# Performance work log

Hardware: AMD Instinct MI355X
Metric: run time of the kernel (lower is better)

The kernel has to match this reference:

```python
import jax, jax.numpy as jnp
import numpy as np

NU, NI, DIN, DH, L, NNZ = 100000, 50000, 64, 128, 2, 5000000
SLOPE = 0.2  # LeakyReLU negative slope (args['p'])
EPS = 1e-5


def setup_inputs() -> dict:
    key = jax.random.key(0)
    ks = jax.random.split(key, 10)
    return {
        'emb_table': jax.random.normal(ks[0], (NU + NI, DIN), jnp.float32) * 0.1,
        'fc_u_w': jax.random.normal(ks[1], (DH, DIN), jnp.float32) * 0.01,
        'fc_u_b': jnp.zeros((DH,), jnp.float32),
        'fc_i_w': jax.random.normal(ks[2], (DH, DIN), jnp.float32) * 0.01,
        'fc_i_b': jnp.zeros((DH,), jnp.float32),
        'vals': jax.random.uniform(ks[3], (NNZ,), jnp.float32),
        'Wu': jax.random.normal(ks[4], (L, DH, DH), jnp.float32) * 0.01,
        'ln1g_u': jnp.ones((L, DH), jnp.float32),
        'ln1b_u': jnp.zeros((L, DH), jnp.float32),
        'ln2g_u': jnp.ones((L, DH), jnp.float32),
        'ln2b_u': jnp.zeros((L, DH), jnp.float32),
        'Wi': jax.random.normal(ks[5], (L, DH, DH), jnp.float32) * 0.01,
        'ln1g_i': jnp.ones((L, DH), jnp.float32),
        'ln1b_i': jnp.zeros((L, DH), jnp.float32),
        'ln2g_i': jnp.ones((L, DH), jnp.float32),
        'ln2b_i': jnp.zeros((L, DH), jnp.float32),
        'rows': jax.random.randint(ks[6], (NNZ,), 0, NU, jnp.int32),
        'cols': jax.random.randint(ks[7], (NNZ,), 0, NI, jnp.int32),
    }


def layer_norm(x, g, b):
    mu = jnp.mean(x, axis=-1, keepdims=True)
    xc = x - mu
    var = jnp.mean(xc * xc, axis=-1, keepdims=True)
    return xc * jax.lax.rsqrt(var + EPS) * g + b


def spmm(r, c, vals, x, n_out):
    # out[r] += vals * x[c]   (sparse [n_out, n_c] @ dense [n_c, d])
    return jax.ops.segment_sum(vals[:, None] * x[c], r, num_segments=n_out)


def hconv(r, c, vals, n_r, n_c, x, W, g1, b1, g2, b2):
    # HGNNConv: ln1(fc(spmm(A^T, x))) then leaky(ln2(spmm(A, lat1)))
    y1 = spmm(c, r, vals, x, n_c)            # [n_c, DH] = A^T x
    lat1 = layer_norm(y1 @ W.T, g1, b1)       # fc bias=False
    y2 = spmm(r, c, vals, lat1, n_r)          # [n_r, DH] = A lat1
    return jax.nn.leaky_relu(layer_norm(y2, g2, b2), SLOPE)


def reference(emb_table, fc_u_w, fc_u_b, fc_i_w, fc_i_b, vals,
              Wu, ln1g_u, ln1b_u, ln2g_u, ln2b_u,
              Wi, ln1g_i, ln1b_i, ln2g_i, ln2b_i,
              rows, cols):
    leaky = lambda x: jax.nn.leaky_relu(x, SLOPE)
    # dropout is identity in eval mode
    u = leaky(emb_table[:NU] @ fc_u_w.T + fc_u_b)   # [NU, DH]
    i = leaky(emb_table[NU:] @ fc_i_w.T + fc_i_b)   # [NI, DH]
    acc = jnp.concatenate([u, i], axis=0)
    for k in range(L):
        hu = hconv(rows, cols, vals, NU, NI, u,
                   Wu[k], ln1g_u[k], ln1b_u[k], ln2g_u[k], ln2b_u[k])
        hi = hconv(cols, rows, vals, NI, NU, i,
                   Wi[k], ln1g_i[k], ln1b_i[k], ln2g_i[k], ln2b_i[k])
        u = u + hu
        i = i + hi
        acc = acc + jnp.concatenate([hu, hi], axis=0)
    all_emb = acc / jnp.float32(L + 1)  # mean over stacked layer outputs
    return all_emb[:NU], all_emb[NU:]
```

## Files before the change

### kernel.cpp

```cpp
#include <hip/hip_runtime.h>
#include <math.h>

namespace {

constexpr int kNU = 100000;
constexpr int kNI = 50000;
constexpr int kDIN = 64;
constexpr int kDH = 128;
constexpr int kDH2 = kDH / 2;
constexpr int kNNZ = 5000000;
constexpr float kSlope = 0.2f;
constexpr float kEps = 1e-5f;

constexpr int kNSeg = kNU + kNI;
constexpr int kScanTile = 2048;
constexpr int kScanBlocks = (kNSeg + kScanTile - 1) / kScanTile;

struct alignas(8) Edge { int idx; float val; };

__device__ inline float2 bf2f(uint p) {
  return make_float2(__uint_as_float(p << 16),
                     __uint_as_float(p & 0xffff0000u));
}
__device__ inline uint f2bf1(float f) {
  const uint a = __float_as_uint(f);
  return (a + 0x7fffu + ((a >> 16) & 1u)) >> 16;
}
__device__ inline uint f2bf(float2 v) {
  return f2bf1(v.x) | (f2bf1(v.y) << 16);
}

__global__ __launch_bounds__(128) void fc_in_kernel(
    const float* __restrict__ emb, const float* __restrict__ wu,
    const float* __restrict__ bu, const float* __restrict__ wi,
    const float* __restrict__ bi, uint* __restrict__ ubuf,
    uint* __restrict__ ibuf, float* __restrict__ out) {
  const int n = blockIdx.x;
  const int d = threadIdx.x;
  __shared__ float e[kDIN];
  __shared__ float sh[kDH];
  if (d < kDIN) e[d] = emb[(size_t)n * kDIN + d];
  __syncthreads();
  const float* W;
  const float* B;
  uint* dst;
  int nl;
  if (n < kNU) { W = wu; B = bu; dst = ubuf; nl = n; }
  else         { W = wi; B = bi; dst = ibuf; nl = n - kNU; }
  float s = B[d];
  const float* wr = W + (size_t)d * kDIN;
#pragma unroll
  for (int k = 0; k < kDIN; ++k) s = fmaf(e[k], wr[k], s);
  s = s > 0.f ? s : kSlope * s;
  sh[d] = s;
  out[(size_t)n * kDH + d] = s;
  __syncthreads();
  if (d < kDH2)
    dst[(size_t)nl * kDH2 + d] = f2bf(make_float2(sh[2 * d], sh[2 * d + 1]));
}

__global__ __launch_bounds__(256) void hist_kernel(
    const int* __restrict__ rows, const int* __restrict__ cols,
    int* __restrict__ cnt) {
  const int e = blockIdx.x * 256 + threadIdx.x;
  if (e >= kNNZ) return;
  atomicAdd(&cnt[rows[e]], 1);
  atomicAdd(&cnt[kNU + cols[e]], 1);
}

__global__ __launch_bounds__(256) void scan_partial_kernel(
    const int* __restrict__ in, int* __restrict__ out, int* __restrict__ bsum,
    int N) {
  __shared__ int sdata[256];
  const int tid = threadIdx.x;
  const int base = blockIdx.x * kScanTile + tid * 8;
  int v[8];
  int s = 0;
#pragma unroll
  for (int j = 0; j < 8; ++j) {
    v[j] = (base + j < N) ? in[base + j] : 0;
    s += v[j];
  }
  sdata[tid] = s;
  __syncthreads();
#pragma unroll
  for (int off = 1; off < 256; off <<= 1) {
    int t = (tid >= off) ? sdata[tid - off] : 0;
    __syncthreads();
    sdata[tid] += t;
    __syncthreads();
  }
  int run = sdata[tid] - s;
#pragma unroll
  for (int j = 0; j < 8; ++j) {
    if (base + j < N) out[base + j] = run;
    run += v[j];
  }
  if (tid == 255) bsum[blockIdx.x] = sdata[255];
}

__global__ __launch_bounds__(256) void scan_bsums_kernel(int* __restrict__ bsum,
                                                         int M) {
  __shared__ int sd[256];
  const int tid = threadIdx.x;
  const int v = (tid < M) ? bsum[tid] : 0;
  sd[tid] = v;
  __syncthreads();
#pragma unroll
  for (int off = 1; off < 256; off <<= 1) {
    int t = (tid >= off) ? sd[tid - off] : 0;
    __syncthreads();
    sd[tid] += t;
    __syncthreads();
  }
  if (tid < M) bsum[tid] = sd[tid] - v;
}

__global__ __launch_bounds__(256) void scan_add_kernel(
    int* __restrict__ out, const int* __restrict__ bsum, int N) {
  const int i = blockIdx.x * 256 + threadIdx.x;
  if (i < N) out[i] += bsum[i / kScanTile];
  if (i == 0) out[N] = 2 * kNNZ;
}

__global__ __launch_bounds__(256) void scatter_kernel(
    const int* __restrict__ rows, const int* __restrict__ cols,
    const float* __restrict__ vals, int* __restrict__ cur,
    Edge* __restrict__ edges) {
  const int e = blockIdx.x * 256 + threadIdx.x;
  if (e >= kNNZ) return;
  const int r = rows[e];
  const int c = cols[e];
  const float v = vals[e];
  const int p = atomicAdd(&cur[r], 1);
  *(int2*)&edges[p] = make_int2(c, __float_as_int(v));
  const int q = atomicAdd(&cur[kNU + c], 1);
  *(int2*)&edges[q] = make_int2(r, __float_as_int(v));
}

__global__ __launch_bounds__(256) void spmm_g1_kernel(
    uint* __restrict__ dst, const uint* __restrict__ src,
    const int* __restrict__ ptr, const Edge* __restrict__ edges, int N) {
  const int wid = threadIdx.x >> 6;
  const int lane = threadIdx.x & 63;
  const int n = blockIdx.x * 4 + wid;
  if (n >= N) return;
  int e = ptr[n];
  const int e1 = ptr[n + 1];
  float2 acc = make_float2(0.f, 0.f);
  for (; e + 4 <= e1; e += 4) {
    const Edge r0 = edges[e + 0];
    const Edge r1 = edges[e + 1];
    const Edge r2 = edges[e + 2];
    const Edge r3 = edges[e + 3];
    const float2 s0 = bf2f(src[(size_t)r0.idx * kDH2 + lane]);
    const float2 s1 = bf2f(src[(size_t)r1.idx * kDH2 + lane]);
    const float2 s2 = bf2f(src[(size_t)r2.idx * kDH2 + lane]);
    const float2 s3 = bf2f(src[(size_t)r3.idx * kDH2 + lane]);
    acc.x = fmaf(r0.val, s0.x, acc.x); acc.y = fmaf(r0.val, s0.y, acc.y);
    acc.x = fmaf(r1.val, s1.x, acc.x); acc.y = fmaf(r1.val, s1.y, acc.y);
    acc.x = fmaf(r2.val, s2.x, acc.x); acc.y = fmaf(r2.val, s2.y, acc.y);
    acc.x = fmaf(r3.val, s3.x, acc.x); acc.y = fmaf(r3.val, s3.y, acc.y);
  }
  for (; e < e1; ++e) {
    const Edge r = edges[e];
    const float2 s = bf2f(src[(size_t)r.idx * kDH2 + lane]);
    acc.x = fmaf(r.val, s.x, acc.x);
    acc.y = fmaf(r.val, s.y, acc.y);
  }
  dst[(size_t)n * kDH2 + lane] = f2bf(acc);
}

__global__ __launch_bounds__(256) void spmm_g2_kernel(
    uint* __restrict__ dstA, const uint* __restrict__ srcA,
    uint* __restrict__ dstB, const uint* __restrict__ srcB,
    const int* __restrict__ ptr, const Edge* __restrict__ edges, int N) {
  const int wid = threadIdx.x >> 6;
  const int lane = threadIdx.x & 63;
  const int n = blockIdx.x * 4 + wid;
  if (n >= N) return;
  int e = ptr[n];
  const int e1 = ptr[n + 1];
  float2 aA = make_float2(0.f, 0.f);
  float2 aB = make_float2(0.f, 0.f);
  for (; e + 4 <= e1; e += 4) {
    const Edge r0 = edges[e + 0];
    const Edge r1 = edges[e + 1];
    const Edge r2 = edges[e + 2];
    const Edge r3 = edges[e + 3];
    const float2 a0 = bf2f(srcA[(size_t)r0.idx * kDH2 + lane]);
    const float2 b0 = bf2f(srcB[(size_t)r0.idx * kDH2 + lane]);
    const float2 a1 = bf2f(srcA[(size_t)r1.idx * kDH2 + lane]);
    const float2 b1 = bf2f(srcB[(size_t)r1.idx * kDH2 + lane]);
    const float2 a2 = bf2f(srcA[(size_t)r2.idx * kDH2 + lane]);
    const float2 b2 = bf2f(srcB[(size_t)r2.idx * kDH2 + lane]);
    const float2 a3 = bf2f(srcA[(size_t)r3.idx * kDH2 + lane]);
    const float2 b3 = bf2f(srcB[(size_t)r3.idx * kDH2 + lane]);
    aA.x = fmaf(r0.val, a0.x, aA.x); aA.y = fmaf(r0.val, a0.y, aA.y);
    aB.x = fmaf(r0.val, b0.x, aB.x); aB.y = fmaf(r0.val, b0.y, aB.y);
    aA.x = fmaf(r1.val, a1.x, aA.x); aA.y = fmaf(r1.val, a1.y, aA.y);
    aB.x = fmaf(r1.val, b1.x, aB.x); aB.y = fmaf(r1.val, b1.y, aB.y);
    aA.x = fmaf(r2.val, a2.x, aA.x); aA.y = fmaf(r2.val, a2.y, aA.y);
    aB.x = fmaf(r2.val, b2.x, aB.x); aB.y = fmaf(r2.val, b2.y, aB.y);
    aA.x = fmaf(r3.val, a3.x, aA.x); aA.y = fmaf(r3.val, a3.y, aA.y);
    aB.x = fmaf(r3.val, b3.x, aB.x); aB.y = fmaf(r3.val, b3.y, aB.y);
  }
  for (; e < e1; ++e) {
    const Edge r = edges[e];
    const float2 a = bf2f(srcA[(size_t)r.idx * kDH2 + lane]);
    const float2 b = bf2f(srcB[(size_t)r.idx * kDH2 + lane]);
    aA.x = fmaf(r.val, a.x, aA.x); aA.y = fmaf(r.val, a.y, aA.y);
    aB.x = fmaf(r.val, b.x, aB.x); aB.y = fmaf(r.val, b.y, aB.y);
  }
  dstA[(size_t)n * kDH2 + lane] = f2bf(aA);
  dstB[(size_t)n * kDH2 + lane] = f2bf(aB);
}

constexpr int kFclnRows = 8;
constexpr int kWPad = 132;

__global__ __launch_bounds__(256) void fcln_kernel(
    const uint* __restrict__ X, const float* __restrict__ W,
    const float* __restrict__ g, const float* __restrict__ b,
    uint* __restrict__ out, int N) {
  __shared__ float Wt[kDH * kWPad];
  __shared__ float Xl[kFclnRows][kDH];
  const int tid = threadIdx.x;
  for (int idx = tid; idx < kDH * kDH; idx += 256) {
    const int d = idx >> 7, k = idx & 127;
    Wt[k * kWPad + d] = W[idx];
  }
  const int row0 = blockIdx.x * kFclnRows;
  const int r = tid >> 5;
  const int l = tid & 31;
  {
    const int n = row0 + r;
    uint2 xv = make_uint2(0u, 0u);
    if (n < N) xv = *(const uint2*)(X + (size_t)n * kDH2 + l * 2);
    const float2 p0 = bf2f(xv.x);
    const float2 p1 = bf2f(xv.y);
    Xl[r][l * 4 + 0] = p0.x;
    Xl[r][l * 4 + 1] = p0.y;
    Xl[r][l * 4 + 2] = p1.x;
    Xl[r][l * 4 + 3] = p1.y;
  }
  __syncthreads();
  float4 acc = make_float4(0.f, 0.f, 0.f, 0.f);
  const int d0 = l * 4;
#pragma unroll 4
  for (int k = 0; k < kDH; ++k) {
    const float x = Xl[r][k];
    const float4 w = *(const float4*)(&Wt[k * kWPad + d0]);
    acc.x = fmaf(x, w.x, acc.x);
    acc.y = fmaf(x, w.y, acc.y);
    acc.z = fmaf(x, w.z, acc.z);
    acc.w = fmaf(x, w.w, acc.w);
  }
  float s = acc.x + acc.y + acc.z + acc.w;
  float sq = acc.x * acc.x + acc.y * acc.y + acc.z * acc.z + acc.w * acc.w;
#pragma unroll
  for (int m = 16; m >= 1; m >>= 1) {
    s += __shfl_xor(s, m, 32);
    sq += __shfl_xor(sq, m, 32);
  }
  const float mu = s * (1.f / kDH);
  const float var = sq * (1.f / kDH) - mu * mu;
  const float rs = 1.f / sqrtf(var + kEps);
  const int n = row0 + r;
  if (n < N) {
    const float4 gg = *(const float4*)(g + d0);
    const float4 bb = *(const float4*)(b + d0);
    float2 o0, o1;
    o0.x = (acc.x - mu) * rs * gg.x + bb.x;
    o0.y = (acc.y - mu) * rs * gg.y + bb.y;
    o1.x = (acc.z - mu) * rs * gg.z + bb.z;
    o1.y = (acc.w - mu) * rs * gg.w + bb.w;
    *(uint2*)(out + (size_t)n * kDH2 + l * 2) = make_uint2(f2bf(o0), f2bf(o1));
  }
}

__global__ __launch_bounds__(256) void leaky_ln_kernel(
    const uint* __restrict__ T, const float* __restrict__ g,
    const float* __restrict__ b, uint* __restrict__ upd,
    float* __restrict__ acc, int N) {
  const int wid = threadIdx.x >> 6;
  const int lane = threadIdx.x & 63;
  const int n = blockIdx.x * 4 + wid;
  if (n >= N) return;
  const float2 v = bf2f(T[(size_t)n * kDH2 + lane]);
  float s = v.x + v.y;
  float sq = v.x * v.x + v.y * v.y;
#pragma unroll
  for (int m = 32; m >= 1; m >>= 1) {
    s += __shfl_xor(s, m, 64);
    sq += __shfl_xor(sq, m, 64);
  }
  const float mu = s * (1.f / kDH);
  const float var = sq * (1.f / kDH) - mu * mu;
  const float rs = 1.f / sqrtf(var + kEps);
  const int d = lane * 2;
  const float2 gg = *(const float2*)(g + d);
  const float2 bb = *(const float2*)(b + d);
  float hx = (v.x - mu) * rs * gg.x + bb.x;
  float hy = (v.y - mu) * rs * gg.y + bb.y;
  hx = hx > 0.f ? hx : kSlope * hx;
  hy = hy > 0.f ? hy : kSlope * hy;
  float2 uv = bf2f(upd[(size_t)n * kDH2 + lane]);
  uv.x += hx;
  uv.y += hy;
  upd[(size_t)n * kDH2 + lane] = f2bf(uv);
  float2 av = *(const float2*)(acc + (size_t)n * kDH + d);
  av.x += hx;
  av.y += hy;
  *(float2*)(acc + (size_t)n * kDH + d) = av;
}

__global__ __launch_bounds__(256) void scale_kernel(float* __restrict__ p,
                                                    float sc, int n4) {
  const int gid = blockIdx.x * 256 + threadIdx.x;
  if (gid < n4) {
    float4 v = ((float4*)p)[gid];
    v.x *= sc; v.y *= sc; v.z *= sc; v.w *= sc;
    ((float4*)p)[gid] = v;
  }
}

}

extern "C" void kernel_launch(void* const* d_in, const int* in_sizes, int n_in,
                              void* d_out, int out_size, void* d_ws,
                              size_t ws_size, hipStream_t stream) {
  const float* emb    = (const float*)d_in[0];
  const float* fc_u_w = (const float*)d_in[1];
  const float* fc_u_b = (const float*)d_in[2];
  const float* fc_i_w = (const float*)d_in[3];
  const float* fc_i_b = (const float*)d_in[4];
  const float* vals   = (const float*)d_in[5];
  const float* Wu     = (const float*)d_in[6];
  const float* ln1g_u = (const float*)d_in[7];
  const float* ln1b_u = (const float*)d_in[8];
  const float* ln2g_u = (const float*)d_in[9];
  const float* ln2b_u = (const float*)d_in[10];
  const float* Wi     = (const float*)d_in[11];
  const float* ln1g_i = (const float*)d_in[12];
  const float* ln1b_i = (const float*)d_in[13];
  const float* ln2g_i = (const float*)d_in[14];
  const float* ln2b_i = (const float*)d_in[15];
  const int*   rows   = (const int*)d_in[16];
  const int*   cols   = (const int*)d_in[17];
  float* out = (float*)d_out;

  uint* bufU = (uint*)d_ws;
  uint* bufI = bufU + (size_t)kNU * kDH2;
  uint* P    = bufI + (size_t)kNI * kDH2;
  uint* Q    = P + (size_t)kNU * kDH2;
  uint* R    = Q + (size_t)kNU * kDH2;
  Edge* edges = (Edge*)(R + (size_t)kNU * kDH2);
  int*  cnt  = (int*)(edges + (size_t)2 * kNNZ);
  int*  ptr  = cnt + kNSeg;
  int*  cur  = ptr + kNSeg + 1;
  int*  bsum = cur + kNSeg + 1;

  const int egrid = (kNNZ + 255) / 256;
  const int gridU = (kNU + 3) / 4;
  const int gridI = (kNI + 3) / 4;
  const int fgridU = (kNU + kFclnRows - 1) / kFclnRows;
  const int fgridI = (kNI + kFclnRows - 1) / kFclnRows;

  hipMemsetAsync(cnt, 0, (size_t)kNSeg * sizeof(int), stream);
  hist_kernel<<<egrid, 256, 0, stream>>>(rows, cols, cnt);
  scan_partial_kernel<<<kScanBlocks, 256, 0, stream>>>(cnt, ptr, bsum, kNSeg);
  scan_bsums_kernel<<<1, 256, 0, stream>>>(bsum, kScanBlocks);
  scan_add_kernel<<<(kNSeg + 255) / 256, 256, 0, stream>>>(ptr, bsum, kNSeg);
  hipMemcpyAsync(cur, ptr, (size_t)(kNSeg + 1) * sizeof(int),
                 hipMemcpyDeviceToDevice, stream);
  scatter_kernel<<<egrid, 256, 0, stream>>>(rows, cols, vals, cur, edges);

  fc_in_kernel<<<kNU + kNI, 128, 0, stream>>>(emb, fc_u_w, fc_u_b, fc_i_w,
                                              fc_i_b, bufU, bufI, out);

  spmm_g1_kernel<<<gridI, 256, 0, stream>>>(P, bufU, ptr + kNU, edges, kNI);
  fcln_kernel<<<fgridI, 256, 0, stream>>>(P, Wu, ln1g_u, ln1b_u, Q, kNI);
  spmm_g2_kernel<<<gridU, 256, 0, stream>>>(P, Q, R, bufI, ptr, edges, kNU);
  leaky_ln_kernel<<<gridU, 256, 0, stream>>>(P, ln2g_u, ln2b_u, bufU, out, kNU);
  fcln_kernel<<<fgridU, 256, 0, stream>>>(R, Wi, ln1g_i, ln1b_i, Q, kNU);
  spmm_g2_kernel<<<gridI, 256, 0, stream>>>(P, Q, R, bufU, ptr + kNU, edges,
                                            kNI);
  leaky_ln_kernel<<<gridI, 256, 0, stream>>>(P, ln2g_i, ln2b_i, bufI,
                                             out + (size_t)kNU * kDH, kNI);
  fcln_kernel<<<fgridI, 256, 0, stream>>>(R, Wu + kDH * kDH, ln1g_u + kDH,
                                          ln1b_u + kDH, Q, kNI);
  spmm_g2_kernel<<<gridU, 256, 0, stream>>>(P, Q, R, bufI, ptr, edges, kNU);
  leaky_ln_kernel<<<gridU, 256, 0, stream>>>(P, ln2g_u + kDH, ln2b_u + kDH,
                                             bufU, out, kNU);
  fcln_kernel<<<fgridU, 256, 0, stream>>>(R, Wi + kDH * kDH, ln1g_i + kDH,
                                          ln1b_i + kDH, Q, kNU);
  spmm_g1_kernel<<<gridI, 256, 0, stream>>>(P, Q, ptr + kNU, edges, kNI);
  leaky_ln_kernel<<<gridI, 256, 0, stream>>>(P, ln2g_i + kDH, ln2b_i + kDH,
                                             bufI, out + (size_t)kNU * kDH,
                                             kNI);

  const int n4 = (kNU + kNI) * kDH / 4;
  scale_kernel<<<(n4 + 255) / 256, 256, 0, stream>>>(out, 1.f / 3.f, n4);
}
```

Baseline: 3.474 ms.

## Replace atomic CSR scatter with two-pass bucketed binning through staging buffer

The single-pass scatter, which did two global atomics and two random 8-byte writes per edge, becomes a two-pass radix-style build. The first pass bins each chunk of edges into 256-segment buckets in shared memory and writes them to a staging buffer in contiguous runs. The second pass places each bucket's edges using shared-memory atomics, so writes land in a localized range. This trades global atomic contention and scattered writes for an extra read and write of a 10M-record staging buffer, which aliases workspace later used by bufU and its neighbours.

```diff
diff --git a/kernel.cpp b/kernel.cpp
--- a/kernel.cpp
+++ b/kernel.cpp
@@ -15,6 +15,11 @@
 constexpr int kNSeg = kNU + kNI;
 constexpr int kScanTile = 2048;
 constexpr int kScanBlocks = (kNSeg + kScanTile - 1) / kScanTile;
+
+constexpr int kBktShift = 8;
+constexpr int kNBkt = (kNSeg + 255) >> kBktShift;
+constexpr int kP1Edges = 3072;
+constexpr int kP1Rec = kP1Edges * 2;
 
 struct alignas(8) Edge { int idx; float val; };
 
@@ -123,19 +128,100 @@
   if (i == 0) out[N] = 2 * kNNZ;
 }
 
-__global__ __launch_bounds__(256) void scatter_kernel(
+__global__ __launch_bounds__(256) void init_gcur_kernel(
+    int* __restrict__ gcur, const int* __restrict__ ptr) {
+  const int b = blockIdx.x * 256 + threadIdx.x;
+  if (b < kNBkt) gcur[b] = ptr[b << kBktShift];
+}
+
+__global__ __launch_bounds__(256) void p1_bin_kernel(
     const int* __restrict__ rows, const int* __restrict__ cols,
-    const float* __restrict__ vals, int* __restrict__ cur,
+    const float* __restrict__ vals, int* __restrict__ gcur,
+    uint2* __restrict__ staging) {
+  __shared__ uint2 rec[kP1Rec];
+  __shared__ int offs[kNBkt + 1];
+  __shared__ int slot[kNBkt];
+  __shared__ int sc[256];
+  const int tid = threadIdx.x;
+  const int e0 = blockIdx.x * kP1Edges;
+  const int ne = min(kP1Edges, kNNZ - e0);
+
+  for (int b = tid; b <= kNBkt; b += 256) offs[b] = 0;
+  __syncthreads();
+  for (int j = tid; j < ne; j += 256) {
+    const int r = rows[e0 + j];
+    const int c = cols[e0 + j];
+    atomicAdd(&offs[r >> kBktShift], 1);
+    atomicAdd(&offs[(kNU + c) >> kBktShift], 1);
+  }
+  __syncthreads();
+  const int base = tid * 3;
+  int v0 = 0, v1 = 0, v2 = 0;
+  if (base + 0 < kNBkt) v0 = offs[base + 0];
+  if (base + 1 < kNBkt) v1 = offs[base + 1];
+  if (base + 2 < kNBkt) v2 = offs[base + 2];
+  const int tsum = v0 + v1 + v2;
+  sc[tid] = tsum;
+  __syncthreads();
+#pragma unroll
+  for (int off = 1; off < 256; off <<= 1) {
+    int t = (tid >= off) ? sc[tid - off] : 0;
+    __syncthreads();
+    sc[tid] += t;
+    __syncthreads();
+  }
+  const int run = sc[tid] - tsum;
+  __syncthreads();
+  if (base + 0 < kNBkt) { offs[base + 0] = run;           slot[base + 0] = run; }
+  if (base + 1 < kNBkt) { offs[base + 1] = run + v0;      slot[base + 1] = run + v0; }
+  if (base + 2 < kNBkt) { offs[base + 2] = run + v0 + v1; slot[base + 2] = run + v0 + v1; }
+  if (tid == 255) offs[kNBkt] = sc[255];
+  __syncthreads();
+  for (int j = tid; j < ne; j += 256) {
+    const int r = rows[e0 + j];
+    const int c = cols[e0 + j];
+    const uint vb = __float_as_uint(vals[e0 + j]);
+    int b = r >> kBktShift;
+    int p = atomicAdd(&slot[b], 1);
+    rec[p] = make_uint2(((uint)c << 8) | (uint)(r & 255), vb);
+    const int s2 = kNU + c;
+    b = s2 >> kBktShift;
+    p = atomicAdd(&slot[b], 1);
+    rec[p] = make_uint2(((uint)r << 8) | (uint)(s2 & 255), vb);
+  }
+  __syncthreads();
+  const int wid = tid >> 6;
+  const int lane = tid & 63;
+  for (int b = wid; b < kNBkt; b += 4) {
+    const int o = offs[b];
+    const int csize = offs[b + 1] - o;
+    if (csize == 0) continue;
+    int gb;
+    if (lane == 0) gb = atomicAdd(&gcur[b], csize);
+    gb = __shfl(gb, 0, 64);
+    for (int r = lane; r < csize; r += 64) staging[gb + r] = rec[o + r];
+  }
+}
+
+__global__ __launch_bounds__(256) void p2_place_kernel(
+    const uint2* __restrict__ staging, const int* __restrict__ ptr,
     Edge* __restrict__ edges) {
-  const int e = blockIdx.x * 256 + threadIdx.x;
-  if (e >= kNNZ) return;
-  const int r = rows[e];
-  const int c = cols[e];
-  const float v = vals[e];
-  const int p = atomicAdd(&cur[r], 1);
-  *(int2*)&edges[p] = make_int2(c, __float_as_int(v));
-  const int q = atomicAdd(&cur[kNU + c], 1);
-  *(int2*)&edges[q] = make_int2(r, __float_as_int(v));
+  __shared__ int curr[256];
+  const int b = blockIdx.x;
+  const int seg0 = b << kBktShift;
+  const int segend = min(seg0 + 256, kNSeg);
+  const int tid = threadIdx.x;
+  if (seg0 + tid < segend) curr[tid] = ptr[seg0 + tid];
+  __syncthreads();
+  const int rbeg = ptr[seg0];
+  const int rend = ptr[segend];
+  for (int r = rbeg + tid; r < rend; r += 256) {
+    const uint2 rc = staging[r];
+    const int sl = rc.x & 255u;
+    const int idx = rc.x >> 8;
+    const int p = atomicAdd(&curr[sl], 1);
+    *(int2*)&edges[p] = make_int2(idx, (int)rc.y);
+  }
 }
 
 __global__ __launch_bounds__(256) void spmm_g1_kernel(
@@ -355,11 +441,12 @@
   uint* P    = bufI + (size_t)kNI * kDH2;
   uint* Q    = P + (size_t)kNU * kDH2;
   uint* R    = Q + (size_t)kNU * kDH2;
+  uint2* staging = (uint2*)d_ws;
   Edge* edges = (Edge*)(R + (size_t)kNU * kDH2);
   int*  cnt  = (int*)(edges + (size_t)2 * kNNZ);
   int*  ptr  = cnt + kNSeg;
-  int*  cur  = ptr + kNSeg + 1;
-  int*  bsum = cur + kNSeg + 1;
+  int*  bsum = ptr + kNSeg + 1;
+  int*  gcur = bsum + kScanBlocks;
 
   const int egrid = (kNNZ + 255) / 256;
   const int gridU = (kNU + 3) / 4;
@@ -372,9 +459,10 @@
   scan_partial_kernel<<<kScanBlocks, 256, 0, stream>>>(cnt, ptr, bsum, kNSeg);
   scan_bsums_kernel<<<1, 256, 0, stream>>>(bsum, kScanBlocks);
   scan_add_kernel<<<(kNSeg + 255) / 256, 256, 0, stream>>>(ptr, bsum, kNSeg);
-  hipMemcpyAsync(cur, ptr, (size_t)(kNSeg + 1) * sizeof(int),
-                 hipMemcpyDeviceToDevice, stream);
-  scatter_kernel<<<egrid, 256, 0, stream>>>(rows, cols, vals, cur, edges);
+  init_gcur_kernel<<<(kNBkt + 255) / 256, 256, 0, stream>>>(gcur, ptr);
+  p1_bin_kernel<<<(kNNZ + kP1Edges - 1) / kP1Edges, 256, 0, stream>>>(
+      rows, cols, vals, gcur, staging);
+  p2_place_kernel<<<kNBkt, 256, 0, stream>>>(staging, ptr, edges);
 
   fc_in_kernel<<<kNU + kNI, 128, 0, stream>>>(emb, fc_u_w, fc_u_b, fc_i_w,
                                               fc_i_b, bufU, bufI, out);
```

Result: slower. 4.339 ms (+24.9%).
